# Kernel optimization log

Hardware: AMD Instinct MI355X
Metric: run time of the kernel (lower is better)

Reference implementation:

```python
import jax, jax.numpy as jnp
import numpy as np


def setup_inputs() -> dict:
    key = jax.random.key(0)
    k1, k2, k3 = jax.random.split(key, 3)
    B, C, T = 16, 256, 1024
    inp = jax.random.normal(k1, (B, C, T), dtype=jnp.float32)
    tgt = jax.random.normal(k2, (B, C, T), dtype=jnp.float32)
    mask = jax.random.uniform(k3, (B, T), dtype=jnp.float32)
    return {"inp": inp, "tgt": tgt, "mask": mask}


def reference(inp, tgt, mask):
    # inp, tgt: (B, C, T); mask: (B, T)
    # permute(0,2,1) -> (B, T, C), then mask along T
    x = jnp.transpose(inp, (0, 2, 1)) * mask[:, :, None]  # (B, T, C)
    y = jnp.transpose(tgt, (0, 2, 1)) * mask[:, :, None]  # (B, T, C)
    xy = jnp.einsum('btc,bsc->bts', x, y)  # (B, T, T)
    xx = jnp.einsum('btc,bsc->bts', x, x)  # (B, T, T)
    yy = jnp.einsum('btc,bsc->bts', y, y)  # (B, T, T)
    similarity = 2.0 * xy / (xx + yy)
    loss = jnp.exp(-similarity)
    return jnp.mean(loss)
```

## Files before the change

kernel.cpp:

```cpp
#include <hip/hip_runtime.h>

constexpr int Bc = 16;
constexpr int Cc = 256;
constexpr int Tc = 1024;

typedef __attribute__((ext_vector_type(16))) float f32x16;

__global__ void zero_out_kernel(float* out) { out[0] = 0.0f; }

__device__ inline unsigned f2fp8(float x) {
    unsigned u = __float_as_uint(x);
    unsigned sign = (u >> 24) & 0x80u;
    unsigned au = u & 0x7fffffffu;
    if (au < 0x3c800000u) {
        float m = __uint_as_float(au) * 512.0f;
        unsigned d = (unsigned)(m + 0.5f);
        return (d > 7u) ? (sign | 0x08u) : (sign | d);
    }
    if (au > 0x43e00000u) au = 0x43e00000u;
    au += 0x7ffffu + ((au >> 20) & 1u);
    unsigned e = (au >> 23) - 120u;
    return sign | (e << 3) | ((au >> 20) & 7u);
}

__global__ __launch_bounds__(256) void convert_fp8_kernel(
    const float* __restrict__ inp, const float* __restrict__ tgt,
    unsigned char* __restrict__ PX, unsigned char* __restrict__ PY,
    float* __restrict__ out)
{
    if (blockIdx.x == 0 && threadIdx.x == 0) out[0] = 0.0f;

    __shared__ float tile[32][132];
    const int gid = blockIdx.x;
    const int a  = gid >> 10;
    const int b  = (gid >> 6) & 15;
    const int cs = (gid >> 3) & 7;
    const int tg = gid & 7;
    const int t0 = tg * 128;
    const int tid = threadIdx.x;

    const float* src = a ? tgt : inp;
    unsigned char* dst = a ? PY : PX;

#pragma unroll
    for (int i = 0; i < 4; ++i) {
        const int c  = i * 8 + (tid >> 5);
        const int t4 = (tid & 31) * 4;
        const float4 v = *(const float4*)&src[((size_t)(b * Cc + cs * 32 + c)) * Tc + t0 + t4];
        tile[c][t4 + 0] = v.x; tile[c][t4 + 1] = v.y;
        tile[c][t4 + 2] = v.z; tile[c][t4 + 3] = v.w;
    }
    __syncthreads();

    const int tb  = tid >> 6;
    const int kh  = (tid >> 5) & 1;
    const int row = tid & 31;
    const int t   = tb * 32 + row;
    unsigned un[4];
#pragma unroll
    for (int q = 0; q < 4; ++q) {
        unsigned wv = 0;
#pragma unroll
        for (int jj = 0; jj < 4; ++jj) {
            const int j  = q * 4 + jj;
            const int cp = kh * 8 + (j & 7) + (j >> 3) * 16;
            wv |= f2fp8(tile[cp][t]) << (jj * 8);
        }
        un[q] = wv;
    }
    const size_t off = ((size_t)((b * 8 + cs) * 32 + tg * 4 + tb)) * 1024
                     + kh * 512 + row * 16;
    *(uint4*)(dst + off) = make_uint4(un[0], un[1], un[2], un[3]);
}

#define GLDS16(g, l) __builtin_amdgcn_global_load_lds(               \
    (__attribute__((address_space(1))) void*)(g),                    \
    (__attribute__((address_space(3))) void*)(l), 16, 0, 0)

#define MF(a, b, c) c = __builtin_amdgcn_mfma_f32_32x32x16_fp8_fp8((a), (b), (c), 0, 0, 0)

__device__ inline float epi_sum(const f32x16& XY, const f32x16& SS) {
    float l = 0.0f;
#pragma unroll
    for (int i = 0; i < 16; ++i) {
        float s = 2.0f * XY[i] / SS[i];
        s = fminf(fmaxf(s, -60.0f), 60.0f);
        l += __expf(-s);
    }
    return l;
}

__global__ __launch_bounds__(256, 4) void jvs_fp8_kernel(
    const unsigned char* __restrict__ PX,
    const unsigned char* __restrict__ PY,
    float* __restrict__ out)
{
    __shared__ __align__(16) unsigned char lds[2][12288];

    const int xcd = blockIdx.x & 7;
    const int idx = blockIdx.x >> 3;
    const int b   = xcd * 2 + (idx >> 7);
    const int r   = idx & 127;
    const int tg  = r >> 4;
    const int sg  = r & 15;

    const int tid  = threadIdx.x;
    const int lane = tid & 63;
    const int w    = tid >> 6;
    const int wm   = w >> 1;
    const int wn   = w & 1;

    const unsigned char* gaxt = PX + ((size_t)(b * 256 + tg * 4 + (tid >> 6))) * 1024
                                   + (tid & 63) * 16;
    const unsigned char* gayt = PY + ((size_t)(b * 256 + tg * 4 + (tid >> 6))) * 1024
                                   + (tid & 63) * 16;
    const unsigned char* gb   = ((tid < 128) ? PX : PY)
                              + ((size_t)(b * 256 + sg * 2 + ((tid & 127) >> 6))) * 1024
                              + (tid & 63) * 16;

    const int fo = (lane >> 5) * 512 + (lane & 31) * 16;

    f32x16 z;
#pragma unroll
    for (int i = 0; i < 16; ++i) z[i] = 0.0f;
    f32x16 xy0 = z, xy1 = z, ss0 = z, ss1 = z;

#define STAGE(bufi, cs)                                               \
    do {                                                              \
        unsigned char* L = lds[bufi];                                 \
        const size_t o = (size_t)(cs) * 32768;                        \
        GLDS16(gaxt + o, L +        tid * 16);                        \
        GLDS16(gayt + o, L + 4096 + tid * 16);                        \
        GLDS16(gb   + o, L + 8192 + tid * 16);                        \
    } while (0)

    STAGE(0, 0);
    __syncthreads();

    for (int it = 0; it < 8; ++it) {
        if (it < 7) STAGE((it + 1) & 1, it + 1);
        const unsigned char* L = lds[it & 1];

        const long2 ax0 = *(const long2*)&L[(2 * wm + 0) * 1024 + fo];
        const long2 ax1 = *(const long2*)&L[(2 * wm + 1) * 1024 + fo];
        const long2 ay0 = *(const long2*)&L[4096 + (2 * wm + 0) * 1024 + fo];
        const long2 ay1 = *(const long2*)&L[4096 + (2 * wm + 1) * 1024 + fo];
        const long2 bx  = *(const long2*)&L[8192 + wn * 1024 + fo];
        const long2 by  = *(const long2*)&L[10240 + wn * 1024 + fo];

        MF(ax0.x, bx.x, ss0); MF(ax1.x, bx.x, ss1);
        MF(ay0.x, by.x, ss0); MF(ay1.x, by.x, ss1);
        MF(ax0.x, by.x, xy0); MF(ax1.x, by.x, xy1);
        MF(ax0.y, bx.y, ss0); MF(ax1.y, bx.y, ss1);
        MF(ay0.y, by.y, ss0); MF(ay1.y, by.y, ss1);
        MF(ax0.y, by.y, xy0); MF(ax1.y, by.y, xy1);

        __syncthreads();
    }
#undef STAGE

    float local = epi_sum(xy0, ss0) + epi_sum(xy1, ss1);

#pragma unroll
    for (int off = 32; off > 0; off >>= 1)
        local += __shfl_down(local, off, 64);

    float* red = (float*)lds;
    if (lane == 0) red[w] = local;
    __syncthreads();
    if (tid == 0)
        atomicAdd(out, (red[0] + red[1] + red[2] + red[3])
                       * (1.0f / ((float)Bc * (float)Tc * (float)Tc)));
}

constexpr int TILE = 64;
constexpr int KC   = 16;

__global__ __launch_bounds__(256) void jvs_loss_kernel(
    const float* __restrict__ inp, const float* __restrict__ tgt, float* __restrict__ out)
{
    __shared__ float xs_t[KC][TILE];
    __shared__ float xs_s[KC][TILE];
    __shared__ float ys_t[KC][TILE];
    __shared__ float ys_s[KC][TILE];

    constexpr int NT = Tc / TILE;
    const int blk = blockIdx.x;
    const int b   = blk / (NT * NT);
    const int r   = blk % (NT * NT);
    const int t0  = (r / NT) * TILE;
    const int s0  = (r % NT) * TILE;
    const int tid = threadIdx.x;
    const int tx  = tid & 15;
    const int ty  = tid >> 4;
    const int lrow  = tid >> 4;
    const int lcol4 = tid & 15;
    const float* baseI = inp + (size_t)b * Cc * Tc;
    const float* baseT = tgt + (size_t)b * Cc * Tc;

    float acc_xy[4][4] = {{0.f}}, acc_xx[4][4] = {{0.f}}, acc_yy[4][4] = {{0.f}};
    for (int c0 = 0; c0 < Cc; c0 += KC) {
        __syncthreads();
        const size_t rowOff = (size_t)(c0 + lrow) * Tc;
        *(float4*)&xs_t[lrow][lcol4 * 4] = *(const float4*)(baseI + rowOff + t0 + lcol4 * 4);
        *(float4*)&xs_s[lrow][lcol4 * 4] = *(const float4*)(baseI + rowOff + s0 + lcol4 * 4);
        *(float4*)&ys_t[lrow][lcol4 * 4] = *(const float4*)(baseT + rowOff + t0 + lcol4 * 4);
        *(float4*)&ys_s[lrow][lcol4 * 4] = *(const float4*)(baseT + rowOff + s0 + lcol4 * 4);
        __syncthreads();
#pragma unroll
        for (int kc = 0; kc < KC; ++kc) {
            float xt[4], xsv[4], yt[4], ysv[4];
#pragma unroll
            for (int i = 0; i < 4; ++i) {
                xt[i]  = xs_t[kc][ty * 4 + i];  yt[i]  = ys_t[kc][ty * 4 + i];
                xsv[i] = xs_s[kc][tx * 4 + i];  ysv[i] = ys_s[kc][tx * 4 + i];
            }
#pragma unroll
            for (int i = 0; i < 4; ++i)
#pragma unroll
                for (int j = 0; j < 4; ++j) {
                    acc_xy[i][j] += xt[i] * ysv[j];
                    acc_xx[i][j] += xt[i] * xsv[j];
                    acc_yy[i][j] += yt[i] * ysv[j];
                }
        }
    }
    float local = 0.0f;
#pragma unroll
    for (int i = 0; i < 4; ++i)
#pragma unroll
        for (int j = 0; j < 4; ++j) {
            float sim = 2.0f * acc_xy[i][j] / (acc_xx[i][j] + acc_yy[i][j]);
            sim = fminf(fmaxf(sim, -60.0f), 60.0f);
            local += __expf(-sim);
        }
#pragma unroll
    for (int off = 32; off > 0; off >>= 1) local += __shfl_down(local, off, 64);
    __shared__ float red[4];
    if ((tid & 63) == 0) red[tid >> 6] = local;
    __syncthreads();
    if (tid == 0)
        atomicAdd(out, (red[0] + red[1] + red[2] + red[3])
                       * (1.0f / ((float)Bc * (float)Tc * (float)Tc)));
}

extern "C" void kernel_launch(void* const* d_in, const int* in_sizes, int n_in,
                              void* d_out, int out_size, void* d_ws, size_t ws_size,
                              hipStream_t stream) {
    const float* inp = (const float*)d_in[0];
    const float* tgt = (const float*)d_in[1];
    float* out = (float*)d_out;

    const size_t oneP = (size_t)Bc * Cc * Tc;
    if (ws_size >= 2 * oneP) {
        unsigned char* PX = (unsigned char*)d_ws;
        unsigned char* PY = PX + oneP;
        convert_fp8_kernel<<<2048, 256, 0, stream>>>(inp, tgt, PX, PY, out);
        jvs_fp8_kernel<<<2048, 256, 0, stream>>>(PX, PY, out);
    } else {
        zero_out_kernel<<<1, 1, 0, stream>>>(out);
        jvs_loss_kernel<<<Bc * (Tc / TILE) * (Tc / TILE), 256, 0, stream>>>(inp, tgt, out);
    }
}
```

Measured before the change: 117.5 us.

## Enlarge fp8 MFMA tile to 512 threads, stagger K-chunk order, use fast reciprocal

Doubles the per-block output tile to 128x128 (8 waves, 4 along s), halving the block count, so each staged A tile is reused across more B columns and global/LDS traffic per output drops. Each block starts its K loop at a different chunk phase so concurrently running blocks don't all hit the same memory region. The epilogue division is replaced with a hardware reciprocal multiply. The larger block and 32KB LDS may reduce occupancy per CU, and the reciprocal is slightly less precise.

```diff
diff --git a/kernel.cpp b/kernel.cpp
--- a/kernel.cpp
+++ b/kernel.cpp
@@ -83,42 +83,52 @@
     float l = 0.0f;
 #pragma unroll
     for (int i = 0; i < 16; ++i) {
-        float s = 2.0f * XY[i] / SS[i];
+        float s = 2.0f * XY[i] * __builtin_amdgcn_rcpf(SS[i]);
         s = fminf(fmaxf(s, -60.0f), 60.0f);
         l += __expf(-s);
     }
     return l;
 }
 
-__global__ __launch_bounds__(256, 4) void jvs_fp8_kernel(
+__global__ __launch_bounds__(512, 4) void jvs_fp8_kernel(
     const unsigned char* __restrict__ PX,
     const unsigned char* __restrict__ PY,
     float* __restrict__ out)
 {
-    __shared__ __align__(16) unsigned char lds[2][12288];
+    __shared__ __align__(16) unsigned char lds[2][16384];
 
     const int xcd = blockIdx.x & 7;
     const int idx = blockIdx.x >> 3;
-    const int b   = xcd * 2 + (idx >> 7);
-    const int r   = idx & 127;
-    const int tg  = r >> 4;
-    const int sg  = r & 15;
+    const int b   = xcd * 2 + (idx >> 6);
+    const int r6  = idx & 63;
+    const int tg  = r6 >> 3;
+    const int sg  = r6 & 7;
 
     const int tid  = threadIdx.x;
     const int lane = tid & 63;
     const int w    = tid >> 6;
-    const int wm   = w >> 1;
-    const int wn   = w & 1;
-
-    const unsigned char* gaxt = PX + ((size_t)(b * 256 + tg * 4 + (tid >> 6))) * 1024
-                                   + (tid & 63) * 16;
-    const unsigned char* gayt = PY + ((size_t)(b * 256 + tg * 4 + (tid >> 6))) * 1024
-                                   + (tid & 63) * 16;
-    const unsigned char* gb   = ((tid < 128) ? PX : PY)
-                              + ((size_t)(b * 256 + sg * 2 + ((tid & 127) >> 6))) * 1024
-                              + (tid & 63) * 16;
+    const int wmh  = w >> 2;
+    const int wnq  = w & 3;
+
+    const int phase = ((idx >> 3) + (idx & 7) + xcd) & 7;
+
+    const unsigned char* gsrc[2];
+    unsigned lchunk[2];
+#pragma unroll
+    for (int i = 0; i < 2; ++i) {
+        const int ch  = w * 2 + i;
+        const int arr = ch >> 2;
+        const int mt  = ch & 3;
+        const unsigned char* base = (arr == 0 || arr == 2) ? PX : PY;
+        const int rowt = (arr < 2) ? (tg * 4 + mt) : (sg * 4 + mt);
+        gsrc[i]   = base + ((size_t)(b * 256 + rowt)) * 1024 + lane * 16;
+        lchunk[i] = ch * 1024 + lane * 16;
+    }
 
     const int fo = (lane >> 5) * 512 + (lane & 31) * 16;
+    const int aoff0 = (2 * wmh + 0) * 1024 + fo;
+    const int aoff1 = (2 * wmh + 1) * 1024 + fo;
+    const int boff  = wnq * 1024 + fo;
 
     f32x16 z;
 #pragma unroll
@@ -129,24 +139,23 @@
     do {                                                              \
         unsigned char* L = lds[bufi];                                 \
         const size_t o = (size_t)(cs) * 32768;                        \
-        GLDS16(gaxt + o, L +        tid * 16);                        \
-        GLDS16(gayt + o, L + 4096 + tid * 16);                        \
-        GLDS16(gb   + o, L + 8192 + tid * 16);                        \
+        GLDS16(gsrc[0] + o, L + lchunk[0]);                           \
+        GLDS16(gsrc[1] + o, L + lchunk[1]);                           \
     } while (0)
 
-    STAGE(0, 0);
+    STAGE(0, phase);
     __syncthreads();
 
     for (int it = 0; it < 8; ++it) {
-        if (it < 7) STAGE((it + 1) & 1, it + 1);
+        if (it < 7) STAGE((it + 1) & 1, (it + 1 + phase) & 7);
         const unsigned char* L = lds[it & 1];
 
-        const long2 ax0 = *(const long2*)&L[(2 * wm + 0) * 1024 + fo];
-        const long2 ax1 = *(const long2*)&L[(2 * wm + 1) * 1024 + fo];
-        const long2 ay0 = *(const long2*)&L[4096 + (2 * wm + 0) * 1024 + fo];
-        const long2 ay1 = *(const long2*)&L[4096 + (2 * wm + 1) * 1024 + fo];
-        const long2 bx  = *(const long2*)&L[8192 + wn * 1024 + fo];
-        const long2 by  = *(const long2*)&L[10240 + wn * 1024 + fo];
+        const long2 ax0 = *(const long2*)&L[aoff0];
+        const long2 ax1 = *(const long2*)&L[aoff1];
+        const long2 ay0 = *(const long2*)&L[4096 + aoff0];
+        const long2 ay1 = *(const long2*)&L[4096 + aoff1];
+        const long2 bx  = *(const long2*)&L[8192 + boff];
+        const long2 by  = *(const long2*)&L[12288 + boff];
 
         MF(ax0.x, bx.x, ss0); MF(ax1.x, bx.x, ss1);
         MF(ay0.x, by.x, ss0); MF(ay1.x, by.x, ss1);
@@ -168,9 +177,12 @@
     float* red = (float*)lds;
     if (lane == 0) red[w] = local;
     __syncthreads();
-    if (tid == 0)
-        atomicAdd(out, (red[0] + red[1] + red[2] + red[3])
-                       * (1.0f / ((float)Bc * (float)Tc * (float)Tc)));
+    if (tid == 0) {
+        float s = 0.0f;
+#pragma unroll
+        for (int i = 0; i < 8; ++i) s += red[i];
+        atomicAdd(out, s * (1.0f / ((float)Bc * (float)Tc * (float)Tc)));
+    }
 }
 
 constexpr int TILE = 64;
@@ -256,7 +268,7 @@
         unsigned char* PX = (unsigned char*)d_ws;
         unsigned char* PY = PX + oneP;
         convert_fp8_kernel<<<2048, 256, 0, stream>>>(inp, tgt, PX, PY, out);
-        jvs_fp8_kernel<<<2048, 256, 0, stream>>>(PX, PY, out);
+        jvs_fp8_kernel<<<1024, 512, 0, stream>>>(PX, PY, out);
     } else {
         zero_out_kernel<<<1, 1, 0, stream>>>(out);
         jvs_loss_kernel<<<Bc * (Tc / TILE) * (Tc / TILE), 256, 0, stream>>>(inp, tgt, out);
```

Result: faster. 103.2 us (-12.2%).
